# Kernel optimization log

Measured on AMD Instinct MI355X. Metric: run time of the kernel, lower is better.

The kernel has to match this reference:

```python
import jax, jax.numpy as jnp
import numpy as np

B, L, D = 4, 8192, 1024

def setup_inputs() -> dict:
    key = jax.random.key(0)
    kx, kg, kc = jax.random.split(key, 3)
    scale = 1.0 / np.sqrt(D)  # ~xavier for [D,D]
    return {
        "x": jax.random.normal(kx, (B, L, D), dtype=jnp.float32),
        "Wg": jax.random.normal(kg, (D, D), dtype=jnp.float32) * scale,
        "bg": jnp.ones((D,), dtype=jnp.float32),   # gate bias init = 1.0
        "Wc": jax.random.normal(kc, (D, D), dtype=jnp.float32) * scale,
        "bc": jnp.zeros((D,), dtype=jnp.float32),  # candidate bias init = 0
    }

def _mingru_scan(gates, candidates):
    # Linear recurrence h_t = g_t * h_{t-1} + c_t, h_0 = 0, along axis=1 (L).
    # Associative combine for pairs (a, b) representing h -> a*h + b.
    def combine(e1, e2):
        a1, b1 = e1
        a2, b2 = e2
        return a2 * a1, a2 * b1 + b2
    _, h = jax.lax.associative_scan(combine, (gates, candidates), axis=1)
    return h

def reference(x, Wg, bg, Wc, bc):
    # gate_proj / candidate_proj: y = x @ W.T + b (torch Linear convention)
    gates = jax.nn.sigmoid(jnp.einsum('bld,ed->ble', x, Wg) + bg)
    candidates = jnp.tanh(jnp.einsum('bld,ed->ble', x, Wc) + bc)
    return _mingru_scan(gates, candidates)  # dropout=0 -> identity
```

## Files before the change

kernel.cpp:

```cpp
#include <hip/hip_runtime.h>
#include <math.h>

#define B_ 4
#define L_ 8192
#define D_ 1024
#define M_ (B_ * L_)
#define K_ D_

#define BM 128
#define BN 128
#define BK 32

#define NCH 64
#define CHL 128

typedef short bf16x8 __attribute__((ext_vector_type(8)));
typedef float f32x4 __attribute__((ext_vector_type(4)));

__device__ __forceinline__ unsigned short f2bf(float f) {
    unsigned u = __float_as_uint(f);
    u += 0x7fff + ((u >> 16) & 1);
    return (unsigned short)(u >> 16);
}
__device__ __forceinline__ float bf2f(unsigned short h) {
    return __uint_as_float(((unsigned)h) << 16);
}

__device__ __forceinline__ void async16(const void* g, void* l) {
    __builtin_amdgcn_global_load_lds(
        (const __attribute__((address_space(1))) unsigned int*)g,
        (__attribute__((address_space(3))) unsigned int*)l, 16, 0, 0);
}

__global__ __launch_bounds__(256) void wprep_kernel(
    const float* __restrict__ Wg, const float* __restrict__ Wc,
    unsigned short* __restrict__ Wghi, unsigned short* __restrict__ Wglo,
    unsigned short* __restrict__ Wchi, unsigned short* __restrict__ Wclo)
{
    int idx = (blockIdx.x * 256 + threadIdx.x) * 4;
    const int n = D_ * D_;
    const float* src; unsigned short *dh, *dl; int o;
    if (idx < n) { src = Wg; dh = Wghi; dl = Wglo; o = idx; }
    else         { src = Wc; dh = Wchi; dl = Wclo; o = idx - n; }
    float4 v = *(const float4*)(src + o);
    ushort4 hi, lo;
    hi.x = f2bf(v.x); lo.x = f2bf(v.x - bf2f(hi.x));
    hi.y = f2bf(v.y); lo.y = f2bf(v.y - bf2f(hi.y));
    hi.z = f2bf(v.z); lo.z = f2bf(v.z - bf2f(hi.z));
    hi.w = f2bf(v.w); lo.w = f2bf(v.w - bf2f(hi.w));
    *(ushort4*)(dh + o) = hi;
    *(ushort4*)(dl + o) = lo;
}

__global__ __launch_bounds__(256, 2) void gemm_scan_kernel(
    const float* __restrict__ X,
    const unsigned short* __restrict__ Wghi, const unsigned short* __restrict__ Wglo,
    const unsigned short* __restrict__ Wchi, const unsigned short* __restrict__ Wclo,
    const float* __restrict__ bg, const float* __restrict__ bc,
    float* __restrict__ P_ws, float* __restrict__ h_ws,
    float* __restrict__ carryA, float* __restrict__ carryB)
{
    __shared__ __align__(16) unsigned short sAhi[BM * BK];
    __shared__ __align__(16) unsigned short sAlo[BM * BK];
    __shared__ __align__(16) unsigned short sBghi[BN * BK];
    __shared__ __align__(16) unsigned short sBglo[BN * BK];
    __shared__ __align__(16) unsigned short sBchi[BN * BK];
    __shared__ __align__(16) unsigned short sBclo[BN * BK];
    __shared__ float cw[2][4][16][2];

    const int t = threadIdx.x;
    const int lane = t & 63;
    const int w = t >> 6;
    const int wrow = w >> 1;
    const int wcol = w & 1;
    const int quad = lane >> 4;
    const int l16  = lane & 15;

    const int m0 = blockIdx.x * BM;
    const int n0 = blockIdx.y * BN;

    f32x4 accg[4][4] = {};
    f32x4 accc[4][4] = {};

#pragma unroll 1
    for (int k0 = 0; k0 < K_; k0 += BK) {
        __syncthreads();

#pragma unroll
        for (int p = 0; p < 2; ++p) {
            int o   = t * 16 + p * 4096;
            int row = o >> 6;
            int kc  = (o & 63) >> 1;
            size_t goff = (size_t)(n0 + row) * K_ + k0 + kc;
            async16(Wghi + goff, (char*)sBghi + o);
            async16(Wglo + goff, (char*)sBglo + o);
            async16(Wchi + goff, (char*)sBchi + o);
            async16(Wclo + goff, (char*)sBclo + o);
        }

#pragma unroll
        for (int p = 0; p < 4; ++p) {
            int idx = (p * 256 + t) * 4;
            int row = idx >> 5;
            int k   = idx & 31;
            float4 v = *(const float4*)(X + (size_t)(m0 + row) * K_ + k0 + k);
            ushort4 hi, lo;
            hi.x = f2bf(v.x); lo.x = f2bf(v.x - bf2f(hi.x));
            hi.y = f2bf(v.y); lo.y = f2bf(v.y - bf2f(hi.y));
            hi.z = f2bf(v.z); lo.z = f2bf(v.z - bf2f(hi.z));
            hi.w = f2bf(v.w); lo.w = f2bf(v.w - bf2f(hi.w));
            *(ushort4*)(sAhi + row * BK + k) = hi;
            *(ushort4*)(sAlo + row * BK + k) = lo;
        }

        __syncthreads();

        bf16x8 ahi[4], alo[4];
#pragma unroll
        for (int i = 0; i < 4; ++i) {
            int off = (wrow * 64 + i * 16 + l16) * BK + quad * 8;
            ahi[i] = *(const bf16x8*)(sAhi + off);
            alo[i] = *(const bf16x8*)(sAlo + off);
        }
#pragma unroll
        for (int j = 0; j < 4; ++j) {
            int off = (wcol * 64 + j * 16 + l16) * BK + quad * 8;
            bf16x8 bgh = *(const bf16x8*)(sBghi + off);
            bf16x8 bgl = *(const bf16x8*)(sBglo + off);
            bf16x8 bch = *(const bf16x8*)(sBchi + off);
            bf16x8 bcl = *(const bf16x8*)(sBclo + off);
#pragma unroll
            for (int i = 0; i < 4; ++i) {
                accg[i][j] = __builtin_amdgcn_mfma_f32_16x16x32_bf16(ahi[i], bgh, accg[i][j], 0, 0, 0);
                accg[i][j] = __builtin_amdgcn_mfma_f32_16x16x32_bf16(ahi[i], bgl, accg[i][j], 0, 0, 0);
                accg[i][j] = __builtin_amdgcn_mfma_f32_16x16x32_bf16(alo[i], bgh, accg[i][j], 0, 0, 0);
                accc[i][j] = __builtin_amdgcn_mfma_f32_16x16x32_bf16(ahi[i], bch, accc[i][j], 0, 0, 0);
                accc[i][j] = __builtin_amdgcn_mfma_f32_16x16x32_bf16(ahi[i], bcl, accc[i][j], 0, 0, 0);
                accc[i][j] = __builtin_amdgcn_mfma_f32_16x16x32_bf16(alo[i], bch, accc[i][j], 0, 0, 0);
            }
        }
    }

    const int b   = m0 >> 13;
    const int chk = (m0 & (L_ - 1)) >> 7;

    float RunA[4], RunB[4];
#pragma unroll
    for (int j = 0; j < 4; ++j) {
        const int n = n0 + wcol * 64 + j * 16 + l16;
        const float bgv = bg[n];
        const float bcv = bc[n];
        float Ar = 1.f, Br = 0.f;
#pragma unroll
        for (int i = 0; i < 4; ++i) {
            float P[4], H[4];
            float pp = 1.f, ph = 0.f;
#pragma unroll
            for (int r = 0; r < 4; ++r) {
                float zg = accg[i][j][r] + bgv;
                float zc = accc[i][j][r] + bcv;
                float g = 1.f / (1.f + __expf(-zg));
                float c = tanhf(zc);
                float Pv = (r == 0) ? g : g * pp;
                float Hv = (r == 0) ? c : fmaf(g, ph, c);
                P[r] = Pv; H[r] = Hv; pp = Pv; ph = Hv;
            }
            float Ai = P[3], Bi = H[3];
            float A1 = __shfl(Ai, (lane - 16) & 63);
            float B1 = __shfl(Bi, (lane - 16) & 63);
            if (quad >= 1) { Bi = fmaf(Ai, B1, Bi); Ai *= A1; }
            float A2 = __shfl(Ai, (lane - 32) & 63);
            float B2 = __shfl(Bi, (lane - 32) & 63);
            if (quad >= 2) { Bi = fmaf(Ai, B2, Bi); Ai *= A2; }
            float Ae = __shfl(Ai, (lane - 16) & 63);
            float Be = __shfl(Bi, (lane - 16) & 63);
            if (quad == 0) { Ae = 1.f; Be = 0.f; }
            float Ca = Ae * Ar;
            float Cb = fmaf(Ae, Br, Be);
#pragma unroll
            for (int r = 0; r < 4; ++r) {
                float Pr = P[r];
                accg[i][j][r] = Pr * Ca;
                accc[i][j][r] = fmaf(Pr, Cb, H[r]);
            }
            float Ag  = __shfl(Ai, l16 + 48);
            float Bg2 = __shfl(Bi, l16 + 48);
            Br = fmaf(Ag, Br, Bg2);
            Ar *= Ag;
        }
        RunA[j] = Ar; RunB[j] = Br;
    }

    if (wrow == 0 && quad == 0) {
#pragma unroll
        for (int j = 0; j < 4; ++j) {
            cw[wcol][j][l16][0] = RunA[j];
            cw[wcol][j][l16][1] = RunB[j];
        }
    }
    __syncthreads();
    if (wrow == 1) {
#pragma unroll
        for (int j = 0; j < 4; ++j) {
            float Aw = cw[wcol][j][l16][0];
            float Bw = cw[wcol][j][l16][1];
#pragma unroll
            for (int i = 0; i < 4; ++i) {
#pragma unroll
                for (int r = 0; r < 4; ++r) {
                    float Pe = accg[i][j][r];
                    accc[i][j][r] = fmaf(Pe, Bw, accc[i][j][r]);
                    accg[i][j][r] = Pe * Aw;
                }
            }
            if (quad == 0) {
                const int n = n0 + wcol * 64 + j * 16 + l16;
                size_t co = (((size_t)b * NCH + chk) << 10) + n;
                carryA[co] = RunA[j] * Aw;
                carryB[co] = fmaf(RunA[j], Bw, RunB[j]);
            }
        }
    }

#pragma unroll
    for (int j = 0; j < 4; ++j) {
        const int n = n0 + wcol * 64 + j * 16 + l16;
#pragma unroll
        for (int i = 0; i < 4; ++i) {
#pragma unroll
            for (int r = 0; r < 4; ++r) {
                int m = m0 + wrow * 64 + i * 16 + quad * 4 + r;
                size_t o = ((size_t)m << 10) + n;
                P_ws[o] = accg[i][j][r];
                h_ws[o] = accc[i][j][r];
            }
        }
    }
}

__global__ __launch_bounds__(256) void scan_carry_kernel(
    const float* __restrict__ carryA, float* __restrict__ carryB)
{
    const int idx = blockIdx.x * 256 + threadIdx.x;
    const int b = idx >> 10;
    const int d = idx & (D_ - 1);
    float acc = 0.f;
    for (int k = 0; k < NCH; ++k) {
        const size_t o = (((size_t)b * NCH + k) << 10) + d;
        const float a  = carryA[o];
        const float bb = carryB[o];
        carryB[o] = acc;
        acc = fmaf(a, acc, bb);
    }
}

__global__ __launch_bounds__(256) void scan_apply_kernel(
    const float* __restrict__ P_ws, const float* __restrict__ h_ws,
    const float* __restrict__ carryB, float* __restrict__ out)
{
    const size_t o = ((size_t)blockIdx.x * 256 + threadIdx.x) * 4;
    const int m  = (int)(o >> 10);
    const int d  = (int)(o & (D_ - 1));
    const int b  = m >> 13;
    const int ch = (m & (L_ - 1)) >> 7;
    const float4 hin = *(const float4*)(carryB + ((((size_t)b * NCH + ch) << 10) + d));
    const float4 P = *(const float4*)(P_ws + o);
    const float4 H = *(const float4*)(h_ws + o);
    float4 r;
    r.x = fmaf(P.x, hin.x, H.x);
    r.y = fmaf(P.y, hin.y, H.y);
    r.z = fmaf(P.z, hin.z, H.z);
    r.w = fmaf(P.w, hin.w, H.w);
    *(float4*)(out + o) = r;
}

extern "C" void kernel_launch(void* const* d_in, const int* in_sizes, int n_in,
                              void* d_out, int out_size, void* d_ws, size_t ws_size,
                              hipStream_t stream)
{
    const float* x  = (const float*)d_in[0];
    const float* Wg = (const float*)d_in[1];
    const float* bg = (const float*)d_in[2];
    const float* Wc = (const float*)d_in[3];
    const float* bc = (const float*)d_in[4];
    float* out = (float*)d_out;

    float* ws = (float*)d_ws;
    float* P_ws   = ws;
    float* h_ws   = P_ws + (size_t)M_ * D_;
    float* carryA = h_ws + (size_t)M_ * D_;
    float* carryB = carryA + (size_t)B_ * NCH * D_;
    unsigned short* Wghi = (unsigned short*)(carryB + (size_t)B_ * NCH * D_);
    unsigned short* Wglo = Wghi + (size_t)D_ * D_;
    unsigned short* Wchi = Wglo + (size_t)D_ * D_;
    unsigned short* Wclo = Wchi + (size_t)D_ * D_;

    wprep_kernel<<<(2 * D_ * D_ / 4) / 256, 256, 0, stream>>>(
        Wg, Wc, Wghi, Wglo, Wchi, Wclo);

    gemm_scan_kernel<<<dim3(M_ / BM, D_ / BN), 256, 0, stream>>>(
        x, Wghi, Wglo, Wchi, Wclo, bg, bc, P_ws, h_ws, carryA, carryB);

    scan_carry_kernel<<<(B_ * D_) / 256, 256, 0, stream>>>(carryA, carryB);

    scan_apply_kernel<<<(M_ * (D_ / 4)) / 256, 256, 0, stream>>>(
        P_ws, h_ws, carryB, out);
}
```

Before: 696.9 us.

## Double-buffer weight tiles in LDS and XOR-swizzle shared layouts

```diff
diff --git a/kernel.cpp b/kernel.cpp
--- a/kernel.cpp
+++ b/kernel.cpp
@@ -62,11 +62,7 @@
 {
     __shared__ __align__(16) unsigned short sAhi[BM * BK];
     __shared__ __align__(16) unsigned short sAlo[BM * BK];
-    __shared__ __align__(16) unsigned short sBghi[BN * BK];
-    __shared__ __align__(16) unsigned short sBglo[BN * BK];
-    __shared__ __align__(16) unsigned short sBchi[BN * BK];
-    __shared__ __align__(16) unsigned short sBclo[BN * BK];
-    __shared__ float cw[2][4][16][2];
+    __shared__ __align__(16) unsigned short sB[2][4][BN * BK];
 
     const int t = threadIdx.x;
     const int lane = t & 63;
@@ -79,56 +75,95 @@
     const int m0 = blockIdx.x * BM;
     const int n0 = blockIdx.y * BN;
 
+    const int rsw = (((l16 & 3) ^ ((l16 >> 2) & 3)) << 3);
+    const int kq  = (quad << 3) ^ rsw;
+    const int aws = ((((t >> 3) & 3) ^ ((t >> 5) & 3)) << 3);
+    const int bSrcChunk = (((t & 3) ^ ((t >> 2) & 3) ^ ((t >> 4) & 3)) << 3);
+
+    const unsigned short* const wp[4] = {Wghi, Wglo, Wchi, Wclo};
+
     f32x4 accg[4][4] = {};
     f32x4 accc[4][4] = {};
 
+#pragma unroll
+    for (int p = 0; p < 2; ++p) {
+        const int o   = t * 16 + p * 4096;
+        const int row = (t >> 2) + p * 64;
+        const size_t goff = (size_t)(n0 + row) * K_ + 0 + bSrcChunk;
+#pragma unroll
+        for (int pl = 0; pl < 4; ++pl)
+            async16(wp[pl] + goff, (char*)sB[0][pl] + o);
+    }
+
 #pragma unroll 1
-    for (int k0 = 0; k0 < K_; k0 += BK) {
-        __syncthreads();
-
-#pragma unroll
-        for (int p = 0; p < 2; ++p) {
-            int o   = t * 16 + p * 4096;
-            int row = o >> 6;
-            int kc  = (o & 63) >> 1;
-            size_t goff = (size_t)(n0 + row) * K_ + k0 + kc;
-            async16(Wghi + goff, (char*)sBghi + o);
-            async16(Wglo + goff, (char*)sBglo + o);
-            async16(Wchi + goff, (char*)sBchi + o);
-            async16(Wclo + goff, (char*)sBclo + o);
-        }
-
+    for (int s = 0; s < 32; ++s) {
+        const int k0  = s * BK;
+        const int cur = s & 1;
+
+        asm volatile("" ::: "memory");
+        __builtin_amdgcn_s_barrier();
+        asm volatile("" ::: "memory");
+
+        float4 xv[4];
 #pragma unroll
         for (int p = 0; p < 4; ++p) {
-            int idx = (p * 256 + t) * 4;
-            int row = idx >> 5;
-            int k   = idx & 31;
-            float4 v = *(const float4*)(X + (size_t)(m0 + row) * K_ + k0 + k);
+            const int row = p * 32 + (t >> 3);
+            const int k   = (t & 7) * 4;
+            xv[p] = *(const float4*)(X + (size_t)(m0 + row) * K_ + k0 + k);
+        }
+
+        if (s < 31) {
+#pragma unroll
+            for (int p = 0; p < 2; ++p) {
+                const int o   = t * 16 + p * 4096;
+                const int row = (t >> 2) + p * 64;
+                const size_t goff = (size_t)(n0 + row) * K_ + (k0 + BK) + bSrcChunk;
+#pragma unroll
+                for (int pl = 0; pl < 4; ++pl)
+                    async16(wp[pl] + goff, (char*)sB[cur ^ 1][pl] + o);
+            }
+        }
+
+#pragma unroll
+        for (int p = 0; p < 4; ++p) {
+            const int row = p * 32 + (t >> 3);
+            const int kk  = ((t & 7) * 4) ^ aws;
+            float4 v = xv[p];
             ushort4 hi, lo;
             hi.x = f2bf(v.x); lo.x = f2bf(v.x - bf2f(hi.x));
             hi.y = f2bf(v.y); lo.y = f2bf(v.y - bf2f(hi.y));
             hi.z = f2bf(v.z); lo.z = f2bf(v.z - bf2f(hi.z));
             hi.w = f2bf(v.w); lo.w = f2bf(v.w - bf2f(hi.w));
-            *(ushort4*)(sAhi + row * BK + k) = hi;
-            *(ushort4*)(sAlo + row * BK + k) = lo;
-        }
-
-        __syncthreads();
+            *(ushort4*)(sAhi + row * BK + kk) = hi;
+            *(ushort4*)(sAlo + row * BK + kk) = lo;
+        }
+
+        asm volatile("s_waitcnt lgkmcnt(0)" ::: "memory");
+        asm volatile("s_waitcnt vmcnt(8)" ::: "memory");
+        __builtin_amdgcn_sched_barrier(0);
+
+        __builtin_amdgcn_s_barrier();
+        asm volatile("" ::: "memory");
+
+        const unsigned short* __restrict__ sb0 = sB[cur][0];
+        const unsigned short* __restrict__ sb1 = sB[cur][1];
+        const unsigned short* __restrict__ sb2 = sB[cur][2];
+        const unsigned short* __restrict__ sb3 = sB[cur][3];
 
         bf16x8 ahi[4], alo[4];
 #pragma unroll
         for (int i = 0; i < 4; ++i) {
-            int off = (wrow * 64 + i * 16 + l16) * BK + quad * 8;
+            const int off = (wrow * 64 + i * 16 + l16) * BK + kq;
             ahi[i] = *(const bf16x8*)(sAhi + off);
             alo[i] = *(const bf16x8*)(sAlo + off);
         }
 #pragma unroll
         for (int j = 0; j < 4; ++j) {
-            int off = (wcol * 64 + j * 16 + l16) * BK + quad * 8;
-            bf16x8 bgh = *(const bf16x8*)(sBghi + off);
-            bf16x8 bgl = *(const bf16x8*)(sBglo + off);
-            bf16x8 bch = *(const bf16x8*)(sBchi + off);
-            bf16x8 bcl = *(const bf16x8*)(sBclo + off);
+            const int off = (wcol * 64 + j * 16 + l16) * BK + kq;
+            bf16x8 bgh = *(const bf16x8*)(sb0 + off);
+            bf16x8 bgl = *(const bf16x8*)(sb1 + off);
+            bf16x8 bch = *(const bf16x8*)(sb2 + off);
+            bf16x8 bcl = *(const bf16x8*)(sb3 + off);
 #pragma unroll
             for (int i = 0; i < 4; ++i) {
                 accg[i][j] = __builtin_amdgcn_mfma_f32_16x16x32_bf16(ahi[i], bgh, accg[i][j], 0, 0, 0);
@@ -191,19 +226,22 @@
         RunA[j] = Ar; RunB[j] = Br;
     }
 
+    __syncthreads();
+    float* cwf = (float*)sAhi;
+
     if (wrow == 0 && quad == 0) {
 #pragma unroll
         for (int j = 0; j < 4; ++j) {
-            cw[wcol][j][l16][0] = RunA[j];
-            cw[wcol][j][l16][1] = RunB[j];
+            cwf[(((wcol * 4 + j) * 16 + l16) << 1) + 0] = RunA[j];
+            cwf[(((wcol * 4 + j) * 16 + l16) << 1) + 1] = RunB[j];
         }
     }
     __syncthreads();
     if (wrow == 1) {
 #pragma unroll
         for (int j = 0; j < 4; ++j) {
-            float Aw = cw[wcol][j][l16][0];
-            float Bw = cw[wcol][j][l16][1];
+            float Aw = cwf[(((wcol * 4 + j) * 16 + l16) << 1) + 0];
+            float Bw = cwf[(((wcol * 4 + j) * 16 + l16) << 1) + 1];
 #pragma unroll
             for (int i = 0; i < 4; ++i) {
 #pragma unroll
```

New measurement: 696.9 us. No clear change (-0.0%).
